# Optimization experiments

Measured on AMD Instinct MI355X. Metric: run time of the kernel, lower is better.

## Reference

```python
import jax, jax.numpy as jnp
import numpy as np

B, S, D_MODEL, NHEAD = 1, 512, 512, 8
D_K = D_MODEL // NHEAD
EPS = 1e-6


def _linear(x, w, b):
    # torch nn.Linear: x @ W^T + b
    return x @ w.T + b


def setup_inputs() -> dict:
    key = jax.random.key(0)
    ks = jax.random.split(key, 18)
    inp = {}
    for i, nm in enumerate(["query", "key", "value", "query_sigma", "key_sigma", "value_sigma"]):
        inp[nm] = jax.random.normal(ks[i], (B, S, D_MODEL), dtype=jnp.float32)
    bound = 1.0 / np.sqrt(D_MODEL)
    pnames = ["wq_mu", "bq_mu", "wk_mu", "bk_mu", "wv_mu", "bv_mu",
              "wq_s", "bq_s", "wk_s", "bk_s", "wv_s", "bv_s"]
    for i, nm in enumerate(pnames):
        shape = (D_MODEL, D_MODEL) if nm.startswith("w") else (D_MODEL,)
        inp[nm] = jax.random.uniform(ks[6 + i], shape, dtype=jnp.float32,
                                     minval=-bound, maxval=bound)
    return inp


def reference(query, key, value, query_sigma, key_sigma, value_sigma,
              wq_mu, bq_mu, wk_mu, bk_mu, wv_mu, bv_mu,
              wq_s, bq_s, wk_s, bk_s, wv_s, bv_s):
    b, s, _ = query.shape
    h, dk = NHEAD, D_K
    mu_q = _linear(query, wq_mu, bq_mu).reshape(b, s, h, dk)
    mu_k = _linear(key, wk_mu, bk_mu).reshape(b, s, h, dk)
    mu_v = _linear(value, wv_mu, bv_mu).reshape(b, s, h, dk)
    sg_q = _linear(query_sigma, wq_s, bq_s).reshape(b, s, h, dk)
    sg_k = _linear(key_sigma, wk_s, bk_s).reshape(b, s, h, dk)
    sg_v = _linear(value_sigma, wv_s, bv_s).reshape(b, s, h, dk)

    # Bhattacharyya distance: broadcast to [b, s_q, s_k, h, dk] then reduce dk
    a = sg_q[:, :, None] ** 2 + EPS   # [b, sq, 1, h, dk]
    c = sg_k[:, None, :] ** 2 + EPS   # [b, 1, sk, h, dk]
    term1 = 0.25 * jnp.log(0.25 * (a / c + c / a + 2.0))
    dmu = mu_q[:, :, None] - mu_k[:, None, :]
    term2 = 0.25 * dmu ** 2 / (sg_q[:, :, None] ** 2 + sg_k[:, None, :] ** 2 + EPS)
    dist = (term1 + term2).sum(-1) / np.sqrt(dk)  # [b, sq, sk, h]
    dist = dist.transpose(0, 3, 1, 2)             # [b, h, sq, sk]

    causal = jnp.triu(jnp.ones((s, s), dtype=bool), k=1)
    dist = jnp.where(causal[None, None], -jnp.inf, dist)
    attn = jax.nn.softmax(dist, axis=-1)

    out_mu = jnp.einsum('bhqk,bkhd->bhqd', attn, mu_v)
    out_var = jnp.maximum(jnp.einsum('bhqk,bkhd->bhqd', attn, sg_v ** 2), 0.0)
    out_sigma = jnp.sqrt(out_var + EPS)
    return out_mu, out_sigma
```

## Files before the change

kernel.cpp:

```cpp
#include <hip/hip_runtime.h>
#include <hip/hip_bf16.h>
#include <math.h>

#define SEQ 512
#define DM 512
#define NH 8
#define DKH 64
#define EPSV 1e-6f
#define LN2F 0.6931471805599453f

typedef __attribute__((ext_vector_type(8))) short short8v;
typedef __attribute__((ext_vector_type(8))) unsigned short ushort8v;
typedef __attribute__((ext_vector_type(16))) float f32x16;

__device__ inline unsigned short f2bf(float x) {
  union { float f; unsigned u; } v; v.f = x;
  unsigned r = v.u + 0x7FFFu + ((v.u >> 16) & 1u);
  return (unsigned short)(r >> 16);
}
__device__ inline float bf2f(unsigned short h) {
  union { float f; unsigned u; } v; v.u = ((unsigned)h) << 16;
  return v.f;
}

struct ConvArgs { const float* src[12]; };

__global__ __launch_bounds__(256) void convert_kernel(ConvArgs a,
                                                      unsigned short* __restrict__ pack) {
  const int m = blockIdx.x >> 7;
  const int g = ((blockIdx.x & 127) << 8) + threadIdx.x;
  const int r = g & 31, ko = (g >> 5) & 63, p = g >> 11;
  const float* src = a.src[m] + (p * 32 + r) * DM + ko * 8;
  float4 x0 = *(const float4*)src;
  float4 x1 = *(const float4*)(src + 4);
  float xs[8] = {x0.x, x0.y, x0.z, x0.w, x1.x, x1.y, x1.z, x1.w};
  ushort8v h1, h2, h3;
#pragma unroll
  for (int e = 0; e < 8; ++e) {
    unsigned short a1 = f2bf(xs[e]);
    float r1 = xs[e] - bf2f(a1);
    unsigned short a2 = f2bf(r1);
    float r2 = r1 - bf2f(a2);
    h1[e] = a1; h2[e] = a2; h3[e] = f2bf(r2);
  }
  unsigned short* dh = pack + (size_t)m * 786432 + p * 16384 + ko * 256 + r * 8;
  *(ushort8v*)dh = h1;
  *(ushort8v*)(dh + 262144) = h2;
  *(ushort8v*)(dh + 524288) = h3;
}

struct GemmArgs { const float* bias[6]; float* out[6]; };

__global__ __launch_bounds__(512) void mfma_proj_kernel(const unsigned short* __restrict__ pack,
                                                        GemmArgs ga) {
  const int p = blockIdx.z;
  const int by = blockIdx.y, bx = blockIdx.x;
  const int t = threadIdx.x, l = t & 63, w = t >> 6;
  const int qd = w & 3, kh = w >> 2;
  const int rowblk = qd >> 1, colblk = qd & 1;
  const int r = l & 31, koff = l >> 5;

  const unsigned short* A = pack + (size_t)p * 786432;
  const unsigned short* B = pack + (size_t)(6 + p) * 786432;
  const int pa = by * 2 + rowblk, pb = bx * 2 + colblk;
  const int ko0 = kh * 32 + koff;
  const size_t aoff = (size_t)pa * 16384 + (size_t)ko0 * 256 + r * 8;
  const size_t boff = (size_t)pb * 16384 + (size_t)ko0 * 256 + r * 8;
  const short8v* A1 = (const short8v*)(A + aoff);
  const short8v* A2 = (const short8v*)(A + 262144 + aoff);
  const short8v* A3 = (const short8v*)(A + 524288 + aoff);
  const short8v* B1 = (const short8v*)(B + boff);
  const short8v* B2 = (const short8v*)(B + 262144 + boff);
  const short8v* B3 = (const short8v*)(B + 524288 + boff);

  f32x16 acc = {};
#pragma unroll 2
  for (int s = 0; s < 16; ++s) {
    short8v a1 = A1[(size_t)s * 64];
    short8v a2 = A2[(size_t)s * 64];
    short8v a3 = A3[(size_t)s * 64];
    short8v b1 = B1[(size_t)s * 64];
    short8v b2 = B2[(size_t)s * 64];
    short8v b3 = B3[(size_t)s * 64];
    acc = __builtin_amdgcn_mfma_f32_32x32x16_bf16(a1, b1, acc, 0, 0, 0);
    acc = __builtin_amdgcn_mfma_f32_32x32x16_bf16(a2, b1, acc, 0, 0, 0);
    acc = __builtin_amdgcn_mfma_f32_32x32x16_bf16(a1, b2, acc, 0, 0, 0);
    acc = __builtin_amdgcn_mfma_f32_32x32x16_bf16(a3, b1, acc, 0, 0, 0);
    acc = __builtin_amdgcn_mfma_f32_32x32x16_bf16(a2, b2, acc, 0, 0, 0);
    acc = __builtin_amdgcn_mfma_f32_32x32x16_bf16(a1, b3, acc, 0, 0, 0);
  }

  __shared__ float red[4][32][33];
  if (kh == 1) {
#pragma unroll
    for (int i = 0; i < 16; ++i) {
      int row = (i & 3) + 8 * (i >> 2) + 4 * (l >> 5);
      red[qd][row][r] = acc[i];
    }
  }
  __syncthreads();
  if (kh == 0) {
    const int colg = bx * 64 + colblk * 32 + r;
    const float bias = ga.bias[p][colg];
    float* C = ga.out[p];
    const int rowbase = by * 64 + rowblk * 32;
#pragma unroll
    for (int i = 0; i < 16; ++i) {
      int row = (i & 3) + 8 * (i >> 2) + 4 * (l >> 5);
      C[(size_t)(rowbase + row) * DM + colg] = acc[i] + red[qd][row][r] + bias;
    }
  }
}

__global__ __launch_bounds__(256) void prep_kernel(float* sq, float* sk, float* sv,
                                                   float* La, float* Lc) {
  const int role = blockIdx.y;
  const int gid  = blockIdx.x * 256 + threadIdx.x;
  const int wid  = gid >> 6;
  const int lane = gid & 63;
  float* buf = (role == 0) ? sq : (role == 1) ? sk : sv;
  const int idx = wid * 64 + lane;
  float v = buf[idx];
  float a = fmaf(v, v, (role == 2) ? 0.f : EPSV);
  buf[idx] = a;
  if (role < 2) {
    float l = __logf(a);
#pragma unroll
    for (int o = 32; o; o >>= 1) l += __shfl_xor(l, o, 64);
    if (lane == 0) ((role == 0) ? La : Lc)[wid] = l;
  }
}

__global__ __launch_bounds__(256) void dist_kernel(const float* __restrict__ aq,
                                                   const float* __restrict__ ak,
                                                   const float* __restrict__ mq,
                                                   const float* __restrict__ mk,
                                                   const float* __restrict__ La,
                                                   const float* __restrict__ Lc,
                                                   float* __restrict__ dist) {
  const int blk = blockIdx.x;
  const int h = blk / 136;
  const int tt = blk % 136;
  int qt = (int)((sqrtf(8.f * tt + 1.f) - 1.f) * 0.5f);
  while ((qt + 1) * (qt + 2) / 2 <= tt) ++qt;
  while (qt * (qt + 1) / 2 > tt) --qt;
  const int kt = tt - qt * (qt + 1) / 2;

  __shared__ float aqs[32][68], mqs[32][68], aks[32][68], mks[32][68];
  const int t = threadIdx.x;
#pragma unroll
  for (int i = 0; i < 2; ++i) {
    int idx = t + 256 * i;
    int r = idx >> 4, c4 = idx & 15;
    int gq = (qt * 32 + r) * DM + h * 64 + c4 * 4;
    int gk = (kt * 32 + r) * DM + h * 64 + c4 * 4;
    *(float4*)&aqs[r][c4 * 4] = *(const float4*)&aq[gq];
    *(float4*)&mqs[r][c4 * 4] = *(const float4*)&mq[gq];
    *(float4*)&aks[r][c4 * 4] = *(const float4*)&ak[gk];
    *(float4*)&mks[r][c4 * 4] = *(const float4*)&mk[gk];
  }
  __syncthreads();

  const int qi = t >> 3;
  const int kb = t & 7;
  float accl[4] = {0.f, 0.f, 0.f, 0.f};
  float acct[4] = {0.f, 0.f, 0.f, 0.f};

#pragma unroll 2
  for (int d4 = 0; d4 < 16; ++d4) {
    float4 qa = *(const float4*)&aqs[qi][d4 * 4];
    float4 qm = *(const float4*)&mqs[qi][d4 * 4];
    float qaa[4] = {qa.x, qa.y, qa.z, qa.w};
    float qmm[4] = {qm.x, qm.y, qm.z, qm.w};
#pragma unroll
    for (int j = 0; j < 4; ++j) {
      int ki = kb + 8 * j;
      float4 ca = *(const float4*)&aks[ki][d4 * 4];
      float4 cm = *(const float4*)&mks[ki][d4 * 4];
      float caa[4] = {ca.x, ca.y, ca.z, ca.w};
      float cmm[4] = {cm.x, cm.y, cm.z, cm.w};
#pragma unroll
      for (int e = 0; e < 4; ++e) {
        float s = qaa[e] + caa[e];
        accl[j] += __log2f(s);
        float dm = qmm[e] - cmm[e];
        float rcp = __builtin_amdgcn_rcpf(s - EPSV);
        acct[j] = fmaf(dm * dm, rcp, acct[j]);
      }
    }
  }

  const int qg = qt * 32 + qi;
  const float la = La[qg * 8 + h];
#pragma unroll
  for (int j = 0; j < 4; ++j) {
    int kg = kt * 32 + kb + 8 * j;
    float lc = Lc[kg * 8 + h];
    float dv = (0.5f * LN2F * accl[j] + 0.25f * acct[j]
                - 0.25f * (la + lc) - 32.f * LN2F) * 0.125f;
    dist[(h * SEQ + qg) * SEQ + kg] = dv;
  }
}

__global__ __launch_bounds__(256) void softmax_pack_kernel(const float* __restrict__ dist,
                                                           unsigned short* __restrict__ aPack) {
  const int t = threadIdx.x;
  const int wid = blockIdx.x * 4 + (t >> 6);
  const int l = t & 63;
  const int h = wid >> 9;
  const int q = wid & 511;
  const float* row = dist + (size_t)wid * SEQ;

  float4 v0 = *(const float4*)&row[l * 8];
  float4 v1 = *(const float4*)&row[l * 8 + 4];
  float vals[8] = {v0.x, v0.y, v0.z, v0.w, v1.x, v1.y, v1.z, v1.w};
  float m = -1e30f;
#pragma unroll
  for (int e = 0; e < 8; ++e) {
    vals[e] = (l * 8 + e <= q) ? vals[e] : -1e30f;
    m = fmaxf(m, vals[e]);
  }
#pragma unroll
  for (int o = 32; o; o >>= 1) m = fmaxf(m, __shfl_xor(m, o, 64));
  float ssum = 0.f;
#pragma unroll
  for (int e = 0; e < 8; ++e) {
    float p = (l * 8 + e <= q) ? __expf(vals[e] - m) : 0.f;
    vals[e] = p;
    ssum += p;
  }
#pragma unroll
  for (int o = 32; o; o >>= 1) ssum += __shfl_xor(ssum, o, 64);
  float rs = 1.f / ssum;

  ushort8v hi, lo;
#pragma unroll
  for (int e = 0; e < 8; ++e) {
    float p = vals[e] * rs;
    unsigned short hh = f2bf(p);
    hi[e] = hh;
    lo[e] = f2bf(p - bf2f(hh));
  }
  unsigned short* dst = aPack + (size_t)h * 524288 + (q >> 5) * 16384 + l * 256 + (q & 31) * 8;
  *(ushort8v*)dst = hi;
  *(ushort8v*)(dst + 262144) = lo;
}

__global__ __launch_bounds__(256) void pvpack_kernel(const float* __restrict__ mv,
                                                     const float* __restrict__ sv2,
                                                     unsigned short* __restrict__ vPack) {
  const int h = blockIdx.x >> 1;
  const int mm = blockIdx.x & 1;
  const float* src = (mm == 0) ? mv : sv2;
  __shared__ float tile[64][65];
  const int t = threadIdx.x;
  unsigned short* base = vPack + (size_t)(h * 2 + mm) * 65536;

  for (int k0 = 0; k0 < SEQ; k0 += 64) {
    __syncthreads();
#pragma unroll
    for (int i = 0; i < 4; ++i) {
      int idx = t + 256 * i;
      int r = idx >> 4, c4 = idx & 15;
      float4 v = *(const float4*)&src[(size_t)(k0 + r) * DM + h * 64 + c4 * 4];
      tile[r][c4 * 4 + 0] = v.x; tile[r][c4 * 4 + 1] = v.y;
      tile[r][c4 * 4 + 2] = v.z; tile[r][c4 * 4 + 3] = v.w;
    }
    __syncthreads();
#pragma unroll
    for (int i = 0; i < 2; ++i) {
      int idx = t + 256 * i;
      int d = idx & 63, ko = idx >> 6;
      ushort8v hi, lo;
#pragma unroll
      for (int e = 0; e < 8; ++e) {
        float x = tile[ko * 8 + e][d];
        unsigned short hh = f2bf(x);
        hi[e] = hh;
        lo[e] = f2bf(x - bf2f(hh));
      }
      int koG = (k0 >> 3) + ko;
      unsigned short* dst = base + (d >> 5) * 16384 + koG * 256 + (d & 31) * 8;
      *(ushort8v*)dst = hi;
      *(ushort8v*)(dst + 32768) = lo;
    }
  }
}

__global__ __launch_bounds__(256) void pv_mfma_kernel(const unsigned short* __restrict__ aPack,
                                                      const unsigned short* __restrict__ vPack,
                                                      float* __restrict__ out) {
  const int h = blockIdx.x >> 4;
  const int qt = blockIdx.x & 15;
  const int t = threadIdx.x, l = t & 63, w = t >> 6;
  const int dt = w & 1, mm = w >> 1;

  const unsigned short* aBase = aPack + (size_t)h * 524288 + qt * 16384
                                + (l >> 5) * 256 + (l & 31) * 8;
  const unsigned short* vBase = vPack + (size_t)(h * 2 + mm) * 65536 + dt * 16384
                                + (l >> 5) * 256 + (l & 31) * 8;

  f32x16 acc = {};
  const int nks = 2 * qt + 2;
  for (int s = 0; s < nks; ++s) {
    short8v a1 = *(const short8v*)(aBase + (size_t)s * 512);
    short8v a2 = *(const short8v*)(aBase + 262144 + (size_t)s * 512);
    short8v b1 = *(const short8v*)(vBase + (size_t)s * 512);
    short8v b2 = *(const short8v*)(vBase + 32768 + (size_t)s * 512);
    acc = __builtin_amdgcn_mfma_f32_32x32x16_bf16(a1, b1, acc, 0, 0, 0);
    acc = __builtin_amdgcn_mfma_f32_32x32x16_bf16(a2, b1, acc, 0, 0, 0);
    acc = __builtin_amdgcn_mfma_f32_32x32x16_bf16(a1, b2, acc, 0, 0, 0);
  }

  float* dst = out + ((mm == 0) ? 0 : (size_t)NH * SEQ * DKH);
  const int col = dt * 32 + (l & 31);
#pragma unroll
  for (int i = 0; i < 16; ++i) {
    int qrow = (i & 3) + 8 * (i >> 2) + 4 * (l >> 5);
    int q = qt * 32 + qrow;
    float v = acc[i];
    if (mm) v = sqrtf(fmaxf(v, 0.f) + EPSV);
    dst[((size_t)h * SEQ + q) * DKH + col] = v;
  }
}

extern "C" void kernel_launch(void* const* d_in, const int* in_sizes, int n_in,
                              void* d_out, int out_size, void* d_ws, size_t ws_size,
                              hipStream_t stream) {
  (void)in_sizes; (void)n_in; (void)out_size; (void)ws_size;

  float* ws = (float*)d_ws;
  float* mq = ws;
  float* mk = mq + 262144;
  float* mv = mk + 262144;
  float* sq = mv + 262144;
  float* sk = sq + 262144;
  float* sv = sk + 262144;
  float* La = sv + 262144;
  float* Lc = La + 4096;
  unsigned short* pack = (unsigned short*)(Lc + 4096);
  float* dist = (float*)pack;
  unsigned short* aPack = pack + 4194304;
  unsigned short* vPack = pack + 8388608;

  ConvArgs ca;
  ca.src[0] = (const float*)d_in[0];
  ca.src[1] = (const float*)d_in[1];
  ca.src[2] = (const float*)d_in[2];
  ca.src[3] = (const float*)d_in[3];
  ca.src[4] = (const float*)d_in[4];
  ca.src[5] = (const float*)d_in[5];
  ca.src[6] = (const float*)d_in[6];
  ca.src[7] = (const float*)d_in[8];
  ca.src[8] = (const float*)d_in[10];
  ca.src[9] = (const float*)d_in[12];
  ca.src[10] = (const float*)d_in[14];
  ca.src[11] = (const float*)d_in[16];

  GemmArgs gaArgs;
  gaArgs.bias[0] = (const float*)d_in[7];  gaArgs.out[0] = mq;
  gaArgs.bias[1] = (const float*)d_in[9];  gaArgs.out[1] = mk;
  gaArgs.bias[2] = (const float*)d_in[11]; gaArgs.out[2] = mv;
  gaArgs.bias[3] = (const float*)d_in[13]; gaArgs.out[3] = sq;
  gaArgs.bias[4] = (const float*)d_in[15]; gaArgs.out[4] = sk;
  gaArgs.bias[5] = (const float*)d_in[17]; gaArgs.out[5] = sv;

  convert_kernel<<<12 * 128, 256, 0, stream>>>(ca, pack);

  dim3 ggrid(8, 8, 6);
  mfma_proj_kernel<<<ggrid, 512, 0, stream>>>(pack, gaArgs);

  dim3 qgrid(1024, 3);
  prep_kernel<<<qgrid, 256, 0, stream>>>(sq, sk, sv, La, Lc);

  dist_kernel<<<8 * 136, 256, 0, stream>>>(sq, sk, mq, mk, La, Lc, dist);

  softmax_pack_kernel<<<1024, 256, 0, stream>>>(dist, aPack);

  pvpack_kernel<<<16, 256, 0, stream>>>(mv, sv, vPack);

  pv_mfma_kernel<<<128, 256, 0, stream>>>(aPack, vPack, (float*)d_out);
}
```

Before: 170.7 us.

## Fuse prep into projection epilogue, enlarge dist tiles, merge softmax and V packing

```diff
diff --git a/kernel.cpp b/kernel.cpp
--- a/kernel.cpp
+++ b/kernel.cpp
@@ -107,27 +107,10 @@
 #pragma unroll
     for (int i = 0; i < 16; ++i) {
       int row = (i & 3) + 8 * (i >> 2) + 4 * (l >> 5);
-      C[(size_t)(rowbase + row) * DM + colg] = acc[i] + red[qd][row][r] + bias;
-    }
-  }
-}
-
-__global__ __launch_bounds__(256) void prep_kernel(float* sq, float* sk, float* sv,
-                                                   float* La, float* Lc) {
-  const int role = blockIdx.y;
-  const int gid  = blockIdx.x * 256 + threadIdx.x;
-  const int wid  = gid >> 6;
-  const int lane = gid & 63;
-  float* buf = (role == 0) ? sq : (role == 1) ? sk : sv;
-  const int idx = wid * 64 + lane;
-  float v = buf[idx];
-  float a = fmaf(v, v, (role == 2) ? 0.f : EPSV);
-  buf[idx] = a;
-  if (role < 2) {
-    float l = __logf(a);
-#pragma unroll
-    for (int o = 32; o; o >>= 1) l += __shfl_xor(l, o, 64);
-    if (lane == 0) ((role == 0) ? La : Lc)[wid] = l;
+      float v = acc[i] + red[qd][row][r] + bias;
+      if (p >= 3) v = fmaf(v, v, (p == 5) ? 0.f : EPSV);
+      C[(size_t)(rowbase + row) * DM + colg] = v;
+    }
   }
 }
 
@@ -135,25 +118,24 @@
                                                    const float* __restrict__ ak,
                                                    const float* __restrict__ mq,
                                                    const float* __restrict__ mk,
-                                                   const float* __restrict__ La,
-                                                   const float* __restrict__ Lc,
                                                    float* __restrict__ dist) {
   const int blk = blockIdx.x;
-  const int h = blk / 136;
-  const int tt = blk % 136;
+  const int h = blk / 36;
+  const int tt = blk % 36;
   int qt = (int)((sqrtf(8.f * tt + 1.f) - 1.f) * 0.5f);
   while ((qt + 1) * (qt + 2) / 2 <= tt) ++qt;
   while (qt * (qt + 1) / 2 > tt) --qt;
   const int kt = tt - qt * (qt + 1) / 2;
 
-  __shared__ float aqs[32][68], mqs[32][68], aks[32][68], mks[32][68];
+  __shared__ float aqs[64][68], mqs[64][68], aks[64][68], mks[64][68];
+  __shared__ float lsum[128][2];
   const int t = threadIdx.x;
 #pragma unroll
-  for (int i = 0; i < 2; ++i) {
+  for (int i = 0; i < 4; ++i) {
     int idx = t + 256 * i;
     int r = idx >> 4, c4 = idx & 15;
-    int gq = (qt * 32 + r) * DM + h * 64 + c4 * 4;
-    int gk = (kt * 32 + r) * DM + h * 64 + c4 * 4;
+    int gq = (qt * 64 + r) * DM + h * 64 + c4 * 4;
+    int gk = (kt * 64 + r) * DM + h * 64 + c4 * 4;
     *(float4*)&aqs[r][c4 * 4] = *(const float4*)&aq[gq];
     *(float4*)&mqs[r][c4 * 4] = *(const float4*)&mq[gq];
     *(float4*)&aks[r][c4 * 4] = *(const float4*)&ak[gk];
@@ -161,128 +143,154 @@
   }
   __syncthreads();
 
-  const int qi = t >> 3;
-  const int kb = t & 7;
-  float accl[4] = {0.f, 0.f, 0.f, 0.f};
-  float acct[4] = {0.f, 0.f, 0.f, 0.f};
+  {
+    int row = t >> 1, par = t & 1;
+    const float* src = (row < 64) ? &aqs[row][0] : &aks[row - 64][0];
+    float s = 0.f;
+#pragma unroll
+    for (int d = 0; d < 32; ++d) s += __log2f(src[par * 32 + d]);
+    lsum[row][par] = s;
+  }
+  __syncthreads();
+
+  const int tq = t >> 4, tk = t & 15;
+  float accl[4][4], acct[4][4];
+#pragma unroll
+  for (int i = 0; i < 4; ++i)
+#pragma unroll
+    for (int j = 0; j < 4; ++j) { accl[i][j] = 0.f; acct[i][j] = 0.f; }
 
 #pragma unroll 2
   for (int d4 = 0; d4 < 16; ++d4) {
-    float4 qa = *(const float4*)&aqs[qi][d4 * 4];
-    float4 qm = *(const float4*)&mqs[qi][d4 * 4];
-    float qaa[4] = {qa.x, qa.y, qa.z, qa.w};
-    float qmm[4] = {qm.x, qm.y, qm.z, qm.w};
+    float4 qa[4], qm[4], ka[4], km[4];
+#pragma unroll
+    for (int i = 0; i < 4; ++i) {
+      qa[i] = *(const float4*)&aqs[tq * 4 + i][d4 * 4];
+      qm[i] = *(const float4*)&mqs[tq * 4 + i][d4 * 4];
+    }
 #pragma unroll
     for (int j = 0; j < 4; ++j) {
-      int ki = kb + 8 * j;
-      float4 ca = *(const float4*)&aks[ki][d4 * 4];
-      float4 cm = *(const float4*)&mks[ki][d4 * 4];
-      float caa[4] = {ca.x, ca.y, ca.z, ca.w};
-      float cmm[4] = {cm.x, cm.y, cm.z, cm.w};
-#pragma unroll
-      for (int e = 0; e < 4; ++e) {
-        float s = qaa[e] + caa[e];
-        accl[j] += __log2f(s);
-        float dm = qmm[e] - cmm[e];
-        float rcp = __builtin_amdgcn_rcpf(s - EPSV);
-        acct[j] = fmaf(dm * dm, rcp, acct[j]);
+      ka[j] = *(const float4*)&aks[tk + 16 * j][d4 * 4];
+      km[j] = *(const float4*)&mks[tk + 16 * j][d4 * 4];
+    }
+#pragma unroll
+    for (int i = 0; i < 4; ++i) {
+      float qav[4] = {qa[i].x, qa[i].y, qa[i].z, qa[i].w};
+      float qmv[4] = {qm[i].x, qm[i].y, qm[i].z, qm[i].w};
+#pragma unroll
+      for (int j = 0; j < 4; ++j) {
+        float kav[4] = {ka[j].x, ka[j].y, ka[j].z, ka[j].w};
+        float kmv[4] = {km[j].x, km[j].y, km[j].z, km[j].w};
+#pragma unroll
+        for (int e = 0; e < 4; ++e) {
+          float s = qav[e] + kav[e];
+          accl[i][j] += __log2f(s);
+          float dm = qmv[e] - kmv[e];
+          float rcp = __builtin_amdgcn_rcpf(s - EPSV);
+          acct[i][j] = fmaf(dm * dm, rcp, acct[i][j]);
+        }
       }
     }
   }
 
-  const int qg = qt * 32 + qi;
-  const float la = La[qg * 8 + h];
-#pragma unroll
-  for (int j = 0; j < 4; ++j) {
-    int kg = kt * 32 + kb + 8 * j;
-    float lc = Lc[kg * 8 + h];
-    float dv = (0.5f * LN2F * accl[j] + 0.25f * acct[j]
-                - 0.25f * (la + lc) - 32.f * LN2F) * 0.125f;
-    dist[(h * SEQ + qg) * SEQ + kg] = dv;
-  }
-}
-
-__global__ __launch_bounds__(256) void softmax_pack_kernel(const float* __restrict__ dist,
-                                                           unsigned short* __restrict__ aPack) {
-  const int t = threadIdx.x;
-  const int wid = blockIdx.x * 4 + (t >> 6);
-  const int l = t & 63;
-  const int h = wid >> 9;
-  const int q = wid & 511;
-  const float* row = dist + (size_t)wid * SEQ;
-
-  float4 v0 = *(const float4*)&row[l * 8];
-  float4 v1 = *(const float4*)&row[l * 8 + 4];
-  float vals[8] = {v0.x, v0.y, v0.z, v0.w, v1.x, v1.y, v1.z, v1.w};
-  float m = -1e30f;
-#pragma unroll
-  for (int e = 0; e < 8; ++e) {
-    vals[e] = (l * 8 + e <= q) ? vals[e] : -1e30f;
-    m = fmaxf(m, vals[e]);
-  }
-#pragma unroll
-  for (int o = 32; o; o >>= 1) m = fmaxf(m, __shfl_xor(m, o, 64));
-  float ssum = 0.f;
-#pragma unroll
-  for (int e = 0; e < 8; ++e) {
-    float p = (l * 8 + e <= q) ? __expf(vals[e] - m) : 0.f;
-    vals[e] = p;
-    ssum += p;
-  }
-#pragma unroll
-  for (int o = 32; o; o >>= 1) ssum += __shfl_xor(ssum, o, 64);
-  float rs = 1.f / ssum;
-
-  ushort8v hi, lo;
-#pragma unroll
-  for (int e = 0; e < 8; ++e) {
-    float p = vals[e] * rs;
-    unsigned short hh = f2bf(p);
-    hi[e] = hh;
-    lo[e] = f2bf(p - bf2f(hh));
-  }
-  unsigned short* dst = aPack + (size_t)h * 524288 + (q >> 5) * 16384 + l * 256 + (q & 31) * 8;
-  *(ushort8v*)dst = hi;
-  *(ushort8v*)(dst + 262144) = lo;
-}
-
-__global__ __launch_bounds__(256) void pvpack_kernel(const float* __restrict__ mv,
-                                                     const float* __restrict__ sv2,
-                                                     unsigned short* __restrict__ vPack) {
-  const int h = blockIdx.x >> 1;
-  const int mm = blockIdx.x & 1;
-  const float* src = (mm == 0) ? mv : sv2;
+  const int qg0 = qt * 64 + tq * 4;
+#pragma unroll
+  for (int i = 0; i < 4; ++i) {
+    float la2 = lsum[tq * 4 + i][0] + lsum[tq * 4 + i][1];
+#pragma unroll
+    for (int j = 0; j < 4; ++j) {
+      int kg = kt * 64 + tk + 16 * j;
+      float lc2 = lsum[64 + tk + 16 * j][0] + lsum[64 + tk + 16 * j][1];
+      float dv = (LN2F * (0.5f * accl[i][j] - 0.25f * (la2 + lc2) - 32.f)
+                  + 0.25f * acct[i][j]) * 0.125f;
+      dist[((size_t)(h * SEQ) + qg0 + i) * SEQ + kg] = dv;
+    }
+  }
+}
+
+__global__ __launch_bounds__(256) void softmax_pvpack_kernel(const float* __restrict__ dist,
+                                                             const float* __restrict__ mv,
+                                                             const float* __restrict__ sv2,
+                                                             unsigned short* __restrict__ aPack,
+                                                             unsigned short* __restrict__ vPack) {
   __shared__ float tile[64][65];
   const int t = threadIdx.x;
-  unsigned short* base = vPack + (size_t)(h * 2 + mm) * 65536;
-
-  for (int k0 = 0; k0 < SEQ; k0 += 64) {
-    __syncthreads();
-#pragma unroll
-    for (int i = 0; i < 4; ++i) {
-      int idx = t + 256 * i;
-      int r = idx >> 4, c4 = idx & 15;
-      float4 v = *(const float4*)&src[(size_t)(k0 + r) * DM + h * 64 + c4 * 4];
-      tile[r][c4 * 4 + 0] = v.x; tile[r][c4 * 4 + 1] = v.y;
-      tile[r][c4 * 4 + 2] = v.z; tile[r][c4 * 4 + 3] = v.w;
-    }
-    __syncthreads();
-#pragma unroll
-    for (int i = 0; i < 2; ++i) {
-      int idx = t + 256 * i;
-      int d = idx & 63, ko = idx >> 6;
-      ushort8v hi, lo;
-#pragma unroll
-      for (int e = 0; e < 8; ++e) {
-        float x = tile[ko * 8 + e][d];
-        unsigned short hh = f2bf(x);
-        hi[e] = hh;
-        lo[e] = f2bf(x - bf2f(hh));
+
+  if (blockIdx.x < 1024) {
+    const int wid = blockIdx.x * 4 + (t >> 6);
+    const int l = t & 63;
+    const int h = wid >> 9;
+    const int q = wid & 511;
+    const float* row = dist + (size_t)wid * SEQ;
+
+    float4 v0 = *(const float4*)&row[l * 8];
+    float4 v1 = *(const float4*)&row[l * 8 + 4];
+    float vals[8] = {v0.x, v0.y, v0.z, v0.w, v1.x, v1.y, v1.z, v1.w};
+    float m = -1e30f;
+#pragma unroll
+    for (int e = 0; e < 8; ++e) {
+      vals[e] = (l * 8 + e <= q) ? vals[e] : -1e30f;
+      m = fmaxf(m, vals[e]);
+    }
+#pragma unroll
+    for (int o = 32; o; o >>= 1) m = fmaxf(m, __shfl_xor(m, o, 64));
+    float ssum = 0.f;
+#pragma unroll
+    for (int e = 0; e < 8; ++e) {
+      float p = (l * 8 + e <= q) ? __expf(vals[e] - m) : 0.f;
+      vals[e] = p;
+      ssum += p;
+    }
+#pragma unroll
+    for (int o = 32; o; o >>= 1) ssum += __shfl_xor(ssum, o, 64);
+    float rs = 1.f / ssum;
+
+    ushort8v hi, lo;
+#pragma unroll
+    for (int e = 0; e < 8; ++e) {
+      float p = vals[e] * rs;
+      unsigned short hh = f2bf(p);
+      hi[e] = hh;
+      lo[e] = f2bf(p - bf2f(hh));
+    }
+    unsigned short* dst = aPack + (size_t)h * 524288 + (q >> 5) * 16384 + l * 256 + (q & 31) * 8;
+    *(ushort8v*)dst = hi;
+    *(ushort8v*)(dst + 262144) = lo;
+  } else {
+    const int bb = blockIdx.x - 1024;
+    const int h = bb >> 1;
+    const int mm = bb & 1;
+    const float* src = (mm == 0) ? mv : sv2;
+    unsigned short* base = vPack + (size_t)(h * 2 + mm) * 65536;
+
+    for (int k0 = 0; k0 < SEQ; k0 += 64) {
+      __syncthreads();
+#pragma unroll
+      for (int i = 0; i < 4; ++i) {
+        int idx = t + 256 * i;
+        int r = idx >> 4, c4 = idx & 15;
+        float4 v = *(const float4*)&src[(size_t)(k0 + r) * DM + h * 64 + c4 * 4];
+        tile[r][c4 * 4 + 0] = v.x; tile[r][c4 * 4 + 1] = v.y;
+        tile[r][c4 * 4 + 2] = v.z; tile[r][c4 * 4 + 3] = v.w;
       }
-      int koG = (k0 >> 3) + ko;
-      unsigned short* dst = base + (d >> 5) * 16384 + koG * 256 + (d & 31) * 8;
-      *(ushort8v*)dst = hi;
-      *(ushort8v*)(dst + 32768) = lo;
+      __syncthreads();
+#pragma unroll
+      for (int i = 0; i < 2; ++i) {
+        int idx = t + 256 * i;
+        int d = idx & 63, ko = idx >> 6;
+        ushort8v hi, lo;
+#pragma unroll
+        for (int e = 0; e < 8; ++e) {
+          float x = tile[ko * 8 + e][d];
+          unsigned short hh = f2bf(x);
+          hi[e] = hh;
+          lo[e] = f2bf(x - bf2f(hh));
+        }
+        int koG = (k0 >> 3) + ko;
+        unsigned short* dst = base + (d >> 5) * 16384 + koG * 256 + (d & 31) * 8;
+        *(ushort8v*)dst = hi;
+        *(ushort8v*)(dst + 32768) = lo;
+      }
     }
   }
 }
@@ -336,9 +344,7 @@
   float* sq = mv + 262144;
   float* sk = sq + 262144;
   float* sv = sk + 262144;
-  float* La = sv + 262144;
-  float* Lc = La + 4096;
-  unsigned short* pack = (unsigned short*)(Lc + 4096);
+  unsigned short* pack = (unsigned short*)(sv + 262144);
   float* dist = (float*)pack;
   unsigned short* aPack = pack + 4194304;
   unsigned short* vPack = pack + 8388608;
@@ -370,14 +376,9 @@
   dim3 ggrid(8, 8, 6);
   mfma_proj_kernel<<<ggrid, 512, 0, stream>>>(pack, gaArgs);
 
-  dim3 qgrid(1024, 3);
-  prep_kernel<<<qgrid, 256, 0, stream>>>(sq, sk, sv, La, Lc);
-
-  dist_kernel<<<8 * 136, 256, 0, stream>>>(sq, sk, mq, mk, La, Lc, dist);
-
-  softmax_pack_kernel<<<1024, 256, 0, stream>>>(dist, aPack);
-
-  pvpack_kernel<<<16, 256, 0, stream>>>(mv, sv, vPack);
+  dist_kernel<<<8 * 36, 256, 0, stream>>>(sq, sk, mq, mk, dist);
+
+  softmax_pvpack_kernel<<<1040, 256, 0, stream>>>(dist, mv, sv, aPack, vPack);
 
   pv_mfma_kernel<<<128, 256, 0, stream>>>(aPack, vPack, (float*)d_out);
 }
```

After: 177.6 us. 1.04x slower.
